# Performance work log

Hardware: AMD Instinct MI355X
Metric: run time of the kernel (lower is better)

The kernel has to match this reference:

```python
import jax, jax.numpy as jnp
import numpy as np

B, LATENT = 8192, 1024
NR, NC = 12, 12                      # nb_rows, nb_cols
H0, W0 = NR + 2, NC + 2              # 14x14 after reshape
EPS = 1e-5
SLOPE = 0.01                         # LeakyReLU default


def setup_inputs() -> dict:
    key = jax.random.key(0)
    ks = jax.random.split(key, 9)
    s = 0.05
    return {
        "x": jax.random.normal(ks[0], (B, LATENT), jnp.float32),
        "fc_w": jax.random.normal(ks[1], (H0 * W0 * 36, LATENT), jnp.float32) * s,
        "fc_b": jax.random.normal(ks[2], (H0 * W0 * 36,), jnp.float32) * s,
        "conv_w": jax.random.normal(ks[3], (16, 36, 2, 2), jnp.float32) * s,
        "conv_b": jax.random.normal(ks[4], (16,), jnp.float32) * s,
        "gamma": jnp.ones((16,), jnp.float32),
        "beta": jnp.zeros((16,), jnp.float32),
        # locally-connected weights: (out_ch, in_ch, Hout, Wout, k*k)
        "lw1": jax.random.normal(ks[5], (6, 16, H0 - 1, W0 - 1, 4), jnp.float32) * s,
        "lw2": jax.random.normal(ks[6], (1, 6, H0 - 2, W0 - 2, 4), jnp.float32) * s,
    }


def _leaky(x):
    return jnp.where(x >= 0, x, SLOPE * x)


def _local_conv2(x, w):
    # x: (B,C,H,W); w: (O,C,Ho,Wo,4) with k=2, stride 1, no padding
    Ho, Wo = w.shape[2], w.shape[3]
    patches = jnp.stack(
        [x[:, :, dy:dy + Ho, dx:dx + Wo] for dy in (0, 1) for dx in (0, 1)],
        axis=-1)  # (B,C,Ho,Wo,4)
    return jnp.einsum('bchwk,ochwk->bohw', patches, w)


def reference(x, fc_w, fc_b, conv_w, conv_b, gamma, beta, lw1, lw2):
    # fc -> view(B, H0, W0, 36) -> permute to NCHW
    h = x @ fc_w.T + fc_b
    h = h.reshape(B, H0, W0, 36).transpose(0, 3, 1, 2)  # (B,36,14,14)
    # Conv2d k=2 padding='same' (torch pads bottom/right for even kernels)
    h = jax.lax.conv_general_dilated(
        h, conv_w, window_strides=(1, 1), padding=((0, 1), (0, 1)),
        dimension_numbers=('NCHW', 'OIHW', 'NCHW')) + conv_b[None, :, None, None]
    h = _leaky(h)
    # BatchNorm2d (training mode: batch stats, biased var)
    mu = h.mean(axis=(0, 2, 3), keepdims=True)
    var = h.var(axis=(0, 2, 3), keepdims=True)
    h = (h - mu) * jax.lax.rsqrt(var + EPS)
    h = h * gamma[None, :, None, None] + beta[None, :, None, None]
    # locally-connected stack: 14x14 -> 13x13 -> 12x12
    h = _leaky(_local_conv2(h, lw1))
    return _local_conv2(h, lw2)  # (B,1,12,12)
```

## Files before the change

kernel.cpp:

```cpp
#include <hip/hip_runtime.h>


#define SLOPE 0.01f

typedef __bf16 bf16x8 __attribute__((ext_vector_type(8)));
typedef float f32x4 __attribute__((ext_vector_type(4)));

typedef const __attribute__((address_space(1))) void* gas_ptr;
typedef __attribute__((address_space(3))) void* las_ptr;

__device__ __forceinline__ void load16_to_lds(const void* g, void* l) {
  __builtin_amdgcn_global_load_lds((gas_ptr)g, (las_ptr)l, 16, 0, 0);
}

__device__ __forceinline__ unsigned short f2bf(float f) {
  union { float f; unsigned int u; } v; v.f = f;
  unsigned int r = v.u + 0x7FFFu + ((v.u >> 16) & 1u);
  return (unsigned short)(r >> 16);
}
__device__ __forceinline__ float bfbits2f(unsigned int bits16) {
  union { unsigned int u; float f; } v; v.u = bits16 << 16;
  return v.f;
}
__device__ __forceinline__ float leaky(float v) { return v >= 0.f ? v : SLOPE * v; }

__global__ void k_cast_x(const float* __restrict__ x, unsigned short* __restrict__ xb,
                         float* __restrict__ stats) {
  if (blockIdx.x == 0 && threadIdx.x < 32) stats[threadIdx.x] = 0.f;
  int gid = blockIdx.x * 256 + threadIdx.x;
  const float4* x4 = (const float4*)x;
  float4 a = x4[gid * 2], b = x4[gid * 2 + 1];
  union { unsigned short s[8]; uint4 v; } o;
  o.s[0] = f2bf(a.x); o.s[1] = f2bf(a.y); o.s[2] = f2bf(a.z); o.s[3] = f2bf(a.w);
  o.s[4] = f2bf(b.x); o.s[5] = f2bf(b.y); o.s[6] = f2bf(b.z); o.s[7] = f2bf(b.w);
  ((uint4*)xb)[gid] = o.v;
}

__global__ void k_fold(const float* __restrict__ fc_w, const float* __restrict__ fc_b,
                       const float* __restrict__ conv_w, const float* __restrict__ conv_b,
                       unsigned short* __restrict__ Wc, float* __restrict__ bc) {
  __shared__ float cw[2304];
  int blk = blockIdx.x, og = blockIdx.y, t = threadIdx.x;
  if (blk == 196) {
    if (og != 0) return;
    uint4 z = make_uint4(0, 0, 0, 0);
    uint4* dst = (uint4*)(Wc + 3136 * 1024);
    for (int i = t; i < 8192; i += 256) dst[i] = z;
    for (int i = 3136 + t; i < 3200; i += 256) bc[i] = 0.f;
    return;
  }
  for (int i = t; i < 2304; i += 256) cw[i] = conv_w[i];
  __syncthreads();
  int i0 = blk / 14, j0 = blk - (blk / 14) * 14;
  float acc[4][4];
#pragma unroll
  for (int o = 0; o < 4; o++)
#pragma unroll
    for (int q = 0; q < 4; q++) acc[o][q] = 0.f;
  for (int c = 0; c < 36; c++) {
#pragma unroll
    for (int dy = 0; dy < 2; dy++) {
      int ii = i0 + dy; if (ii > 13) continue;
#pragma unroll
      for (int dx = 0; dx < 2; dx++) {
        int jj = j0 + dx; if (jj > 13) continue;
        int row = (ii * 14 + jj) * 36 + c;
        float4 f = *(const float4*)(fc_w + row * 1024 + t * 4);
        int kk = dy * 2 + dx;
#pragma unroll
        for (int oo = 0; oo < 4; oo++) {
          int o = og * 4 + oo;
          float w = cw[(o * 36 + c) * 4 + kk];
          acc[oo][0] += w * f.x; acc[oo][1] += w * f.y;
          acc[oo][2] += w * f.z; acc[oo][3] += w * f.w;
        }
      }
    }
  }
#pragma unroll
  for (int oo = 0; oo < 4; oo++) {
    int o = og * 4 + oo;
    int n = o * 196 + i0 * 14 + j0;
    union { unsigned short s[4]; uint2 v; } u;
    u.s[0] = f2bf(acc[oo][0]); u.s[1] = f2bf(acc[oo][1]);
    u.s[2] = f2bf(acc[oo][2]); u.s[3] = f2bf(acc[oo][3]);
    *(uint2*)(Wc + n * 1024 + t * 4) = u.v;
  }
  if (og == 0 && t < 16) {
    int o = t;
    float b = conv_b[o];
    for (int c = 0; c < 36; c++)
      for (int dy = 0; dy < 2; dy++) {
        int ii = i0 + dy; if (ii > 13) continue;
        for (int dx = 0; dx < 2; dx++) {
          int jj = j0 + dx; if (jj > 13) continue;
          b += cw[(o * 36 + c) * 4 + dy * 2 + dx] * fc_b[(ii * 14 + jj) * 36 + c];
        }
      }
    bc[o * 196 + i0 * 14 + j0] = b;
  }
}

__global__ __launch_bounds__(256, 4) void k_gemm(const unsigned short* __restrict__ Xb,
                                                 const unsigned short* __restrict__ Wcb,
                                                 const float* __restrict__ bc,
                                                 unsigned short* __restrict__ h2) {
  __shared__ __align__(16) char lds[16384];
  const int t = threadIdx.x;
  const int w = t >> 6, lane = t & 63;
  const int quad = lane >> 4, l15 = lane & 15;
  const int m0 = blockIdx.y * 128, n0 = blockIdx.x * 128;
  const int mrow = t & 127, tko = t >> 7;
  const unsigned short* ga = Xb + (m0 + mrow) * 1024 + tko * 8;
  const unsigned short* gb = Wcb + (n0 + mrow) * 1024 + tko * 8;
  char* lA = lds;
  char* lB = lds + 8192;
  const int wbase = w * 1024;
  const int wm0 = (w >> 1) * 64, wn0 = (w & 1) * 64;

  f32x4 acc[4][4];
#pragma unroll
  for (int a = 0; a < 4; a++)
#pragma unroll
    for (int b = 0; b < 4; b++) acc[a][b] = (f32x4){0.f, 0.f, 0.f, 0.f};

  for (int kb = 0; kb < 1024; kb += 32) {
    __syncthreads();
    load16_to_lds(ga + kb,      lA + wbase);
    load16_to_lds(ga + kb + 16, lA + 4096 + wbase);
    load16_to_lds(gb + kb,      lB + wbase);
    load16_to_lds(gb + kb + 16, lB + 4096 + wbase);
    __syncthreads();

    bf16x8 af[4], bfr[4];
#pragma unroll
    for (int mb = 0; mb < 4; mb++)
      af[mb] = *(const bf16x8*)(lA + quad * 2048 + (wm0 + mb * 16 + l15) * 16);
#pragma unroll
    for (int nb = 0; nb < 4; nb++)
      bfr[nb] = *(const bf16x8*)(lB + quad * 2048 + (wn0 + nb * 16 + l15) * 16);
#pragma unroll
    for (int mb = 0; mb < 4; mb++)
#pragma unroll
      for (int nb = 0; nb < 4; nb++)
        acc[mb][nb] = __builtin_amdgcn_mfma_f32_16x16x32_bf16(af[mb], bfr[nb], acc[mb][nb], 0, 0, 0);
  }

#pragma unroll
  for (int nb = 0; nb < 4; nb++) {
    int col = n0 + wn0 + nb * 16 + l15;
    float bias = bc[col];
#pragma unroll
    for (int mb = 0; mb < 4; mb++) {
#pragma unroll
      for (int r = 0; r < 4; r++) {
        int row = m0 + wm0 + mb * 16 + quad * 4 + r;
        float v = acc[mb][nb][r] + bias;
        h2[row * 3200 + col] = f2bf(leaky(v));
      }
    }
  }
}

__global__ void k_stats(const unsigned short* __restrict__ h2, float* __restrict__ stats) {
  int o = blockIdx.x;
  int b0 = blockIdx.y * 64;
  float s = 0.f, s2 = 0.f;
  for (int i = threadIdx.x; i < 64 * 98; i += 256) {
    int b = i / 98, q = i - b * 98;
    unsigned int u = *(const unsigned int*)(h2 + (b0 + b) * 3200 + o * 196 + q * 2);
    float v0 = bfbits2f(u & 0xffffu), v1 = bfbits2f(u >> 16);
    s += v0 + v1; s2 += v0 * v0 + v1 * v1;
  }
  for (int off = 32; off; off >>= 1) {
    s += __shfl_down(s, off, 64);
    s2 += __shfl_down(s2, off, 64);
  }
  __shared__ float ps[8];
  int wv = threadIdx.x >> 6, lane = threadIdx.x & 63;
  if (lane == 0) { ps[wv * 2] = s; ps[wv * 2 + 1] = s2; }
  __syncthreads();
  if (threadIdx.x == 0) {
    atomicAdd(&stats[o],      ps[0] + ps[2] + ps[4] + ps[6]);
    atomicAdd(&stats[16 + o], ps[1] + ps[3] + ps[5] + ps[7]);
  }
}

__global__ __launch_bounds__(256) void k_tail(const unsigned short* __restrict__ h2,
                                              const float* __restrict__ stats,
                                              const float* __restrict__ gamma,
                                              const float* __restrict__ beta,
                                              const float* __restrict__ lw1,
                                              const float* __restrict__ lw2,
                                              float* __restrict__ out) {
  __shared__ unsigned short h3[4 * 3138];
  __shared__ float h4[4 * 1015];
  __shared__ float sc[16], sh[16];
  int b0 = blockIdx.x * 4, t = threadIdx.x;
  if (t < 16) {
    const float inv = 1.f / 1605632.f;
    float mean = stats[t] * inv;
    float var = stats[16 + t] * inv - mean * mean;
    float rstd = rsqrtf(var + 1e-5f);
    float s = gamma[t] * rstd;
    sc[t] = s; sh[t] = beta[t] - mean * s;
  }
  __syncthreads();
  for (int i = t; i < 6272; i += 256) {
    int bb = i / 1568, q = i - bb * 1568;
    int n = q * 2, o = n / 196;
    unsigned int u = *(const unsigned int*)(h2 + (b0 + bb) * 3200 + n);
    float v0 = bfbits2f(u & 0xffffu) * sc[o] + sh[o];
    float v1 = bfbits2f(u >> 16) * sc[o] + sh[o];
    unsigned int pk = (unsigned int)f2bf(v0) | ((unsigned int)f2bf(v1) << 16);
    *(unsigned int*)(h3 + bb * 3138 + n) = pk;
  }
  __syncthreads();
  for (int u = t; u < 312; u += 256) {
    int bb = u & 3, rest = u >> 2;
    int o = rest / 13, y = rest - o * 13;
    float acc[13];
#pragma unroll
    for (int x = 0; x < 13; x++) acc[x] = 0.f;
    const unsigned short* hb = h3 + bb * 3138;
    for (int c = 0; c < 16; c++) {
      float r0[14], r1[14];
      const unsigned int* p0 = (const unsigned int*)(hb + c * 196 + y * 14);
      const unsigned int* p1 = (const unsigned int*)(hb + c * 196 + (y + 1) * 14);
#pragma unroll
      for (int q = 0; q < 7; q++) {
        unsigned int v0 = p0[q], v1 = p1[q];
        r0[2 * q] = bfbits2f(v0 & 0xffffu); r0[2 * q + 1] = bfbits2f(v0 >> 16);
        r1[2 * q] = bfbits2f(v1 & 0xffffu); r1[2 * q + 1] = bfbits2f(v1 >> 16);
      }
      const float* wp = lw1 + (((o * 16 + c) * 13 + y) * 13) * 4;
#pragma unroll
      for (int x = 0; x < 13; x++)
        acc[x] += r0[x] * wp[x * 4] + r0[x + 1] * wp[x * 4 + 1] +
                  r1[x] * wp[x * 4 + 2] + r1[x + 1] * wp[x * 4 + 3];
    }
#pragma unroll
    for (int x = 0; x < 13; x++)
      h4[bb * 1015 + (o * 13 + y) * 13 + x] = leaky(acc[x]);
  }
  __syncthreads();
  for (int oi = t; oi < 576; oi += 256) {
    int pos = oi >> 2, bb = oi & 3;
    int y = pos / 12, x = pos - y * 12;
    float a = 0.f;
    const float* hp = h4 + bb * 1015;
#pragma unroll
    for (int c = 0; c < 6; c++) {
      const float* wpc = lw2 + ((c * 12 + y) * 12 + x) * 4;
      int hb = c * 169 + y * 13 + x;
      a += hp[hb] * wpc[0] + hp[hb + 1] * wpc[1] +
           hp[hb + 13] * wpc[2] + hp[hb + 14] * wpc[3];
    }
    out[(b0 + bb) * 144 + pos] = a;
  }
}

extern "C" void kernel_launch(void* const* d_in, const int* in_sizes, int n_in,
                              void* d_out, int out_size, void* d_ws, size_t ws_size,
                              hipStream_t stream) {
  const float* x      = (const float*)d_in[0];
  const float* fc_w   = (const float*)d_in[1];
  const float* fc_b   = (const float*)d_in[2];
  const float* conv_w = (const float*)d_in[3];
  const float* conv_b = (const float*)d_in[4];
  const float* gamma  = (const float*)d_in[5];
  const float* beta   = (const float*)d_in[6];
  const float* lw1    = (const float*)d_in[7];
  const float* lw2    = (const float*)d_in[8];

  char* ws = (char*)d_ws;
  unsigned short* Xb    = (unsigned short*)(ws);
  unsigned short* Wc    = (unsigned short*)(ws + 16777216);
  float*          bc    = (float*)(ws + 23330816);
  float*          stats = (float*)(ws + 23343616);
  unsigned short* h2    = (unsigned short*)(ws + 23343744);

  k_cast_x<<<4096, 256, 0, stream>>>(x, Xb, stats);
  k_fold<<<dim3(197, 4), 256, 0, stream>>>(fc_w, fc_b, conv_w, conv_b, Wc, bc);
  k_gemm<<<dim3(25, 64), 256, 0, stream>>>(Xb, Wc, bc, h2);
  k_stats<<<dim3(16, 128), 256, 0, stream>>>(h2, stats);
  k_tail<<<2048, 256, 0, stream>>>(h2, stats, gamma, beta, lw1, lw2, (float*)d_out);
}
```

Before: 412.6 us.

## Double-buffer GEMM LDS, fuse BN stats into GEMM epilogue, vectorize tail weights

The GEMM main loop now uses two LDS buffers, so the next K-slice loads while the current one is multiplied, removing one barrier per iteration. Batch-norm sum and sum-of-squares are computed in the GEMM epilogue from the fp32 values, reduced with wave shuffles and atomically added per channel, which drops the separate k_stats kernel and its re-read of h2. Locally-connected weight loads in k_tail become float4 loads. The changes cost doubled LDS (which may limit occupancy), and the stats now come from fp32 rather than bf16-rounded values, with each tile split across at most two channels.

```diff
diff --git a/kernel.cpp b/kernel.cpp
--- a/kernel.cpp
+++ b/kernel.cpp
@@ -104,8 +104,10 @@
 __global__ __launch_bounds__(256, 4) void k_gemm(const unsigned short* __restrict__ Xb,
                                                  const unsigned short* __restrict__ Wcb,
                                                  const float* __restrict__ bc,
-                                                 unsigned short* __restrict__ h2) {
-  __shared__ __align__(16) char lds[16384];
+                                                 unsigned short* __restrict__ h2,
+                                                 float* __restrict__ stats) {
+  __shared__ __align__(16) char lds[32768];
+  __shared__ float red[4][4];
   const int t = threadIdx.x;
   const int w = t >> 6, lane = t & 63;
   const int quad = lane >> 4, l15 = lane & 15;
@@ -113,8 +115,6 @@
   const int mrow = t & 127, tko = t >> 7;
   const unsigned short* ga = Xb + (m0 + mrow) * 1024 + tko * 8;
   const unsigned short* gb = Wcb + (n0 + mrow) * 1024 + tko * 8;
-  char* lA = lds;
-  char* lB = lds + 8192;
   const int wbase = w * 1024;
   const int wm0 = (w >> 1) * 64, wn0 = (w & 1) * 64;
 
@@ -124,14 +124,17 @@
 #pragma unroll
     for (int b = 0; b < 4; b++) acc[a][b] = (f32x4){0.f, 0.f, 0.f, 0.f};
 
-  for (int kb = 0; kb < 1024; kb += 32) {
-    __syncthreads();
-    load16_to_lds(ga + kb,      lA + wbase);
-    load16_to_lds(ga + kb + 16, lA + 4096 + wbase);
-    load16_to_lds(gb + kb,      lB + wbase);
-    load16_to_lds(gb + kb + 16, lB + 4096 + wbase);
-    __syncthreads();
-
+  auto stage = [&](int buf, int kb) {
+    char* sA = lds + buf * 16384;
+    char* sB = sA + 8192;
+    load16_to_lds(ga + kb,      sA + wbase);
+    load16_to_lds(ga + kb + 16, sA + 4096 + wbase);
+    load16_to_lds(gb + kb,      sB + wbase);
+    load16_to_lds(gb + kb + 16, sB + 4096 + wbase);
+  };
+  auto compute = [&](int buf) {
+    char* lA = lds + buf * 16384;
+    char* lB = lA + 8192;
     bf16x8 af[4], bfr[4];
 #pragma unroll
     for (int mb = 0; mb < 4; mb++)
@@ -144,45 +147,64 @@
 #pragma unroll
       for (int nb = 0; nb < 4; nb++)
         acc[mb][nb] = __builtin_amdgcn_mfma_f32_16x16x32_bf16(af[mb], bfr[nb], acc[mb][nb], 0, 0, 0);
-  }
-
+  };
+
+  stage(0, 0);
+  __syncthreads();
+  int cur = 0;
+  for (int kb = 0; kb < 992; kb += 32) {
+    stage(cur ^ 1, kb + 32);
+    compute(cur);
+    __syncthreads();
+    cur ^= 1;
+  }
+  compute(cur);
+
+  const int cLo = n0 / 196;
+  const int cHi = (n0 + 127) / 196;
+  float ss0 = 0.f, ss1 = 0.f, sq0 = 0.f, sq1 = 0.f;
 #pragma unroll
   for (int nb = 0; nb < 4; nb++) {
     int col = n0 + wn0 + nb * 16 + l15;
     float bias = bc[col];
+    int ch = col / 196;
+    bool hi = (ch != cLo);
+    bool valid = col < 3136;
+    float cs = 0.f, cq = 0.f;
 #pragma unroll
     for (int mb = 0; mb < 4; mb++) {
 #pragma unroll
       for (int r = 0; r < 4; r++) {
         int row = m0 + wm0 + mb * 16 + quad * 4 + r;
-        float v = acc[mb][nb][r] + bias;
-        h2[row * 3200 + col] = f2bf(leaky(v));
-      }
-    }
-  }
-}
-
-__global__ void k_stats(const unsigned short* __restrict__ h2, float* __restrict__ stats) {
-  int o = blockIdx.x;
-  int b0 = blockIdx.y * 64;
-  float s = 0.f, s2 = 0.f;
-  for (int i = threadIdx.x; i < 64 * 98; i += 256) {
-    int b = i / 98, q = i - b * 98;
-    unsigned int u = *(const unsigned int*)(h2 + (b0 + b) * 3200 + o * 196 + q * 2);
-    float v0 = bfbits2f(u & 0xffffu), v1 = bfbits2f(u >> 16);
-    s += v0 + v1; s2 += v0 * v0 + v1 * v1;
-  }
-  for (int off = 32; off; off >>= 1) {
-    s += __shfl_down(s, off, 64);
-    s2 += __shfl_down(s2, off, 64);
-  }
-  __shared__ float ps[8];
-  int wv = threadIdx.x >> 6, lane = threadIdx.x & 63;
-  if (lane == 0) { ps[wv * 2] = s; ps[wv * 2 + 1] = s2; }
-  __syncthreads();
-  if (threadIdx.x == 0) {
-    atomicAdd(&stats[o],      ps[0] + ps[2] + ps[4] + ps[6]);
-    atomicAdd(&stats[16 + o], ps[1] + ps[3] + ps[5] + ps[7]);
+        float v = leaky(acc[mb][nb][r] + bias);
+        h2[row * 3200 + col] = f2bf(v);
+        cs += v; cq += v * v;
+      }
+    }
+    if (valid) {
+      if (hi) { ss1 += cs; sq1 += cq; } else { ss0 += cs; sq0 += cq; }
+    }
+  }
+#pragma unroll
+  for (int off = 1; off < 64; off <<= 1) {
+    ss0 += __shfl_xor(ss0, off, 64);
+    ss1 += __shfl_xor(ss1, off, 64);
+    sq0 += __shfl_xor(sq0, off, 64);
+    sq1 += __shfl_xor(sq1, off, 64);
+  }
+  if (lane == 0) { red[w][0] = ss0; red[w][1] = ss1; red[w][2] = sq0; red[w][3] = sq1; }
+  __syncthreads();
+  if (t == 0) {
+    float a0 = red[0][0] + red[1][0] + red[2][0] + red[3][0];
+    float a1 = red[0][1] + red[1][1] + red[2][1] + red[3][1];
+    float b0 = red[0][2] + red[1][2] + red[2][2] + red[3][2];
+    float b1 = red[0][3] + red[1][3] + red[2][3] + red[3][3];
+    atomicAdd(&stats[cLo], a0);
+    atomicAdd(&stats[16 + cLo], b0);
+    if (cHi != cLo && cHi < 16) {
+      atomicAdd(&stats[cHi], a1);
+      atomicAdd(&stats[16 + cHi], b1);
+    }
   }
 }
 
@@ -233,11 +255,13 @@
         r0[2 * q] = bfbits2f(v0 & 0xffffu); r0[2 * q + 1] = bfbits2f(v0 >> 16);
         r1[2 * q] = bfbits2f(v1 & 0xffffu); r1[2 * q + 1] = bfbits2f(v1 >> 16);
       }
-      const float* wp = lw1 + (((o * 16 + c) * 13 + y) * 13) * 4;
-#pragma unroll
-      for (int x = 0; x < 13; x++)
-        acc[x] += r0[x] * wp[x * 4] + r0[x + 1] * wp[x * 4 + 1] +
-                  r1[x] * wp[x * 4 + 2] + r1[x + 1] * wp[x * 4 + 3];
+      const float4* wp4 = (const float4*)(lw1 + (((o * 16 + c) * 13 + y) * 13) * 4);
+#pragma unroll
+      for (int x = 0; x < 13; x++) {
+        float4 wv = wp4[x];
+        acc[x] += r0[x] * wv.x + r0[x + 1] * wv.y +
+                  r1[x] * wv.z + r1[x + 1] * wv.w;
+      }
     }
 #pragma unroll
     for (int x = 0; x < 13; x++)
@@ -249,12 +273,13 @@
     int y = pos / 12, x = pos - y * 12;
     float a = 0.f;
     const float* hp = h4 + bb * 1015;
+    const float4* w4 = (const float4*)lw2;
 #pragma unroll
     for (int c = 0; c < 6; c++) {
-      const float* wpc = lw2 + ((c * 12 + y) * 12 + x) * 4;
+      float4 wv = w4[(c * 12 + y) * 12 + x];
       int hb = c * 169 + y * 13 + x;
-      a += hp[hb] * wpc[0] + hp[hb + 1] * wpc[1] +
-           hp[hb + 13] * wpc[2] + hp[hb + 14] * wpc[3];
+      a += hp[hb] * wv.x + hp[hb + 1] * wv.y +
+           hp[hb + 13] * wv.z + hp[hb + 14] * wv.w;
     }
     out[(b0 + bb) * 144 + pos] = a;
   }
@@ -282,7 +307,6 @@
 
   k_cast_x<<<4096, 256, 0, stream>>>(x, Xb, stats);
   k_fold<<<dim3(197, 4), 256, 0, stream>>>(fc_w, fc_b, conv_w, conv_b, Wc, bc);
-  k_gemm<<<dim3(25, 64), 256, 0, stream>>>(Xb, Wc, bc, h2);
-  k_stats<<<dim3(16, 128), 256, 0, stream>>>(h2, stats);
+  k_gemm<<<dim3(25, 64), 256, 0, stream>>>(Xb, Wc, bc, h2, stats);
   k_tail<<<2048, 256, 0, stream>>>(h2, stats, gamma, beta, lw1, lw2, (float*)d_out);
 }
```

Measured after the change: 384.9 us. 1.07x faster.
